# Kernel tuning notes

Measured on AMD Instinct MI355X. Metric: run time of the kernel, lower is better.

Reference implementation:

```python
import jax, jax.numpy as jnp
import numpy as np

L, B, E, H = 2048, 2, 1024, 16
D = E // H
R = E // 4  # self-space subspace rank
ALPHA = 0.6


def setup_inputs() -> dict:
    key = jax.random.key(0)
    ks = jax.random.split(key, 11)
    s = 0.02
    return {
        "x": jax.random.normal(ks[0], (L, B, E), jnp.float32),
        "attn_mask": jnp.zeros((L, L), jnp.float32),
        "Wq": jax.random.normal(ks[1], (E, E), jnp.float32) * s,
        "bq": jnp.zeros((E,), jnp.float32),
        "Wk": jax.random.normal(ks[2], (E, E), jnp.float32) * s,
        "bk": jnp.zeros((E,), jnp.float32),
        "Wv": jax.random.normal(ks[3], (E, E), jnp.float32) * s,
        "bv": jnp.zeros((E,), jnp.float32),
        "Wo": jax.random.normal(ks[4], (E, E), jnp.float32) * s,
        "bo": jnp.zeros((E,), jnp.float32),
        "U": jax.random.normal(ks[5], (E, R), jnp.float32) * (1.0 / np.sqrt(E)),
    }


def _condition(t, U):
    # self_space.condition: blend with projection onto learned subspace U
    # t: [..., E]
    return ALPHA * t + (1.0 - ALPHA) * ((t @ U) @ U.T)


def reference(x, attn_mask, Wq, bq, Wk, bk, Wv, bv, Wo, bo, U):
    # x: [L, B, E] (seq-first)
    Q = x @ Wq.T + bq
    K = x @ Wk.T + bk
    V = x @ Wv.T + bv
    Qc = _condition(Q, U)
    Kc = _condition(K, U)
    # split heads: [L, B, H, D]
    q = Qc.reshape(L, B, H, D)
    k = Kc.reshape(L, B, H, D)
    v = V.reshape(L, B, H, D)
    scores = jnp.einsum("lbhd,mbhd->bhlm", q, k) / jnp.sqrt(jnp.float32(D))
    scores = scores + attn_mask  # broadcast [L,L] over [B,H,L,L]
    attn_weights = jax.nn.softmax(scores, axis=-1)  # dropout p=0.0 -> identity
    ctx = jnp.einsum("bhlm,mbhd->lbhd", attn_weights, v).reshape(L, B, E)
    out = ctx @ Wo.T + bo
    return out, attn_weights  # attn_weights: [B, H, L, L]
```

## Files before the change

kernel.cpp:

```cpp
#include <hip/hip_runtime.h>
#include <cstddef>

#define L_SEQ  2048
#define B_SZ   2
#define E_DIM  1024
#define H_N    16
#define D_HEAD 64
#define R_DIM  256

typedef unsigned short u16;
using bf16x8 = __attribute__((ext_vector_type(8))) short;
using f32x4  = __attribute__((ext_vector_type(4))) float;

__device__ __forceinline__ u16 bf16rne(float f) {
    unsigned u = __float_as_uint(f);
    return (u16)((u + 0x7FFFu + ((u >> 16) & 1u)) >> 16);
}
__device__ __forceinline__ float b2f(u16 h) {
    return __uint_as_float(((unsigned)h) << 16);
}

__global__ __launch_bounds__(256)
void convert_hilo(const float* __restrict__ in, u16* __restrict__ hi,
                  u16* __restrict__ lo, int n4)
{
    for (int i = blockIdx.x * 256 + threadIdx.x; i < n4; i += gridDim.x * 256) {
        float4 v = ((const float4*)in)[i];
        u16 h0 = bf16rne(v.x), h1 = bf16rne(v.y), h2 = bf16rne(v.z), h3 = bf16rne(v.w);
        uint2 hp;
        hp.x = (unsigned)h0 | ((unsigned)h1 << 16);
        hp.y = (unsigned)h2 | ((unsigned)h3 << 16);
        ((uint2*)hi)[i] = hp;
        u16 l0 = bf16rne(v.x - b2f(h0)), l1 = bf16rne(v.y - b2f(h1));
        u16 l2 = bf16rne(v.z - b2f(h2)), l3 = bf16rne(v.w - b2f(h3));
        uint2 lp;
        lp.x = (unsigned)l0 | ((unsigned)l1 << 16);
        lp.y = (unsigned)l2 | ((unsigned)l3 << 16);
        ((uint2*)lo)[i] = lp;
    }
}

__global__ __launch_bounds__(256)
void transpose_f32_hilo(const float* __restrict__ in, u16* __restrict__ oh,
                        u16* __restrict__ ol, int rows, int cols)
{
    __shared__ float t[32][33];
    const int tx = threadIdx.x & 31, ty = threadIdx.x >> 5;
    const int r0 = blockIdx.y * 32, c0 = blockIdx.x * 32;
    #pragma unroll
    for (int i = 0; i < 4; i++)
        t[ty + i * 8][tx] = in[(size_t)(r0 + ty + i * 8) * cols + c0 + tx];
    __syncthreads();
    #pragma unroll
    for (int i = 0; i < 4; i++) {
        float v = t[tx][ty + i * 8];
        u16 h = bf16rne(v);
        size_t o = (size_t)(c0 + ty + i * 8) * rows + r0 + tx;
        oh[o] = h;
        ol[o] = bf16rne(v - b2f(h));
    }
}

__global__ __launch_bounds__(256)
void transpose_v_bf16(const u16* __restrict__ vh, u16* __restrict__ vt)
{
    __shared__ u16 t[32][34];
    const int tx = threadIdx.x & 31, ty = threadIdx.x >> 5;
    const int l0 = blockIdx.x * 32, d0 = blockIdx.y * 32;
    const int z = blockIdx.z, b = z >> 4, h = z & 15;
    #pragma unroll
    for (int i = 0; i < 4; i++)
        t[ty + i * 8][tx] =
            vh[(size_t)((l0 + ty + i * 8) * B_SZ + b) * E_DIM + h * D_HEAD + d0 + tx];
    __syncthreads();
    #pragma unroll
    for (int i = 0; i < 4; i++)
        vt[(size_t)(z * D_HEAD + d0 + ty + i * 8) * L_SEQ + l0 + tx] = t[tx][ty + i * 8];
}

__global__ void flag_init(int* f) { if (threadIdx.x == 0) *f = 0; }

__global__ __launch_bounds__(256)
void mask_scan(const float* __restrict__ m, int* __restrict__ f, int n4)
{
    int nz = 0;
    for (int i = blockIdx.x * 256 + threadIdx.x; i < n4; i += gridDim.x * 256) {
        float4 v = ((const float4*)m)[i];
        nz |= (v.x != 0.0f) | (v.y != 0.0f) | (v.z != 0.0f) | (v.w != 0.0f);
    }
    if (nz) atomicOr(f, 1);
}

template <int BN, bool SPLIT, bool AF32>
__global__ __launch_bounds__(256)
void gemm_mfma(const void* __restrict__ Ah_, const void* __restrict__ Al_,
               const u16* __restrict__ Bh_, const u16* __restrict__ Bl_,
               float* __restrict__ Cf, u16* __restrict__ Ch, u16* __restrict__ Cl,
               const u16* __restrict__ Cinh, const u16* __restrict__ Cinl,
               const float* __restrict__ bias,
               int M, int N, int K, int lda, int ldb, int ldc,
               long aStride, int aMode, long bStride, int bMode,
               long cStride, int cMode, float alpha, float beta)
{
    constexpr int BM = 128, BK = 64;
    constexpr int WN = BN / 32;
    constexpr int ALO = BM * BK, BLO = BN * BK;
    __shared__ __align__(16) u16 As[(SPLIT ? 2 : 1) * BM * BK];
    __shared__ __align__(16) u16 Bs[(SPLIT ? 2 : 1) * BN * BK];

    const int tid = threadIdx.x;
    const int z = blockIdx.z;
    const int headOff = (z >> 4) * E_DIM + (z & 15) * D_HEAD;
    const int aOff = aMode ? headOff : (int)(z * aStride);
    const int bOff = bMode ? headOff : (int)(z * bStride);
    const int cOff = cMode ? headOff : (int)(z * cStride);
    const int tm = blockIdx.y * BM, tn = blockIdx.x * BN;

    const int sRow = tid >> 3, sG = tid & 7;
    const int lane = tid & 63;
    const int fr = lane & 15, kg = lane >> 4;
    const int wave = tid >> 6;
    const int wm = (wave >> 1) * 64;
    const int wn = (wave & 1) * (BN / 2);

    f32x4 acc[4][WN] = {};

    for (int k0 = 0; k0 < K; k0 += BK) {
        if constexpr (!AF32) {
            const u16* Ah = (const u16*)Ah_ + aOff + k0;
            #pragma unroll
            for (int i = 0; i < 4; i++) {
                int row = sRow + i * 32;
                int p = sG ^ (row & 7);
                int dst = row * BK + p * 8;
                *(uint4*)&As[dst] = *(const uint4*)(Ah + (tm + row) * lda + sG * 8);
                if constexpr (SPLIT) {
                    const u16* Al = (const u16*)Al_ + aOff + k0;
                    *(uint4*)&As[ALO + dst] = *(const uint4*)(Al + (tm + row) * lda + sG * 8);
                }
            }
        } else {
            const float* Af = (const float*)Ah_ + aOff + k0;
            const int rowF = tid >> 4, qF = tid & 15;
            #pragma unroll
            for (int i = 0; i < 8; i++) {
                int row = rowF + i * 16;
                float4 v = *(const float4*)(Af + (long)(tm + row) * lda + qF * 4);
                int p = (qF >> 1) ^ (row & 7);
                uint2 pk;
                pk.x = (unsigned)bf16rne(v.x) | ((unsigned)bf16rne(v.y) << 16);
                pk.y = (unsigned)bf16rne(v.z) | ((unsigned)bf16rne(v.w) << 16);
                *(uint2*)&As[row * BK + p * 8 + (qF & 1) * 4] = pk;
            }
        }
        {
            const u16* Bh = Bh_ + bOff + k0;
            #pragma unroll
            for (int i = 0; i < BN / 32; i++) {
                int row = sRow + i * 32;
                int p = sG ^ (row & 7);
                int dst = row * BK + p * 8;
                *(uint4*)&Bs[dst] = *(const uint4*)(Bh + (tn + row) * ldb + sG * 8);
                if constexpr (SPLIT) {
                    const u16* Bl = Bl_ + bOff + k0;
                    *(uint4*)&Bs[BLO + dst] = *(const uint4*)(Bl + (tn + row) * ldb + sG * 8);
                }
            }
        }
        __syncthreads();

        #pragma unroll
        for (int ks = 0; ks < 2; ks++) {
            bf16x8 ah[4], al[4];
            #pragma unroll
            for (int m = 0; m < 4; m++) {
                int row = wm + m * 16 + fr;
                int p = (ks * 4 + kg) ^ (row & 7);
                ah[m] = *(const bf16x8*)&As[row * BK + p * 8];
                if constexpr (SPLIT)
                    al[m] = *(const bf16x8*)&As[ALO + row * BK + p * 8];
            }
            #pragma unroll
            for (int n = 0; n < WN; n++) {
                int col = wn + n * 16 + fr;
                int p = (ks * 4 + kg) ^ (col & 7);
                bf16x8 bh = *(const bf16x8*)&Bs[col * BK + p * 8];
                #pragma unroll
                for (int m = 0; m < 4; m++)
                    acc[m][n] = __builtin_amdgcn_mfma_f32_16x16x32_bf16(ah[m], bh, acc[m][n], 0, 0, 0);
                if constexpr (SPLIT) {
                    bf16x8 bl = *(const bf16x8*)&Bs[BLO + col * BK + p * 8];
                    #pragma unroll
                    for (int m = 0; m < 4; m++) {
                        acc[m][n] = __builtin_amdgcn_mfma_f32_16x16x32_bf16(al[m], bh, acc[m][n], 0, 0, 0);
                        acc[m][n] = __builtin_amdgcn_mfma_f32_16x16x32_bf16(ah[m], bl, acc[m][n], 0, 0, 0);
                    }
                }
            }
        }
        __syncthreads();
    }

    #pragma unroll
    for (int m = 0; m < 4; m++) {
        int row0 = tm + wm + m * 16 + kg * 4;
        #pragma unroll
        for (int n = 0; n < WN; n++) {
            int col = tn + wn + n * 16 + fr;
            float bv = bias ? bias[col] : 0.0f;
            #pragma unroll
            for (int j = 0; j < 4; j++) {
                int idx = cOff + (row0 + j) * ldc + col;
                float v = alpha * acc[m][n][j] + bv;
                if (beta != 0.0f) {
                    float ci = b2f(Cinh[idx]);
                    if (Cinl) ci += b2f(Cinl[idx]);
                    v += beta * ci;
                }
                if (Cf) Cf[idx] = v;
                if (Ch) {
                    u16 h = bf16rne(v);
                    Ch[idx] = h;
                    if (Cl) Cl[idx] = bf16rne(v - b2f(h));
                }
            }
        }
    }
}

__global__ __launch_bounds__(256)
void attn_fused(const u16* __restrict__ Qc, const u16* __restrict__ Kc,
                const u16* __restrict__ Vt, float* __restrict__ attn,
                u16* __restrict__ ctxh, u16* __restrict__ ctxl,
                const float* __restrict__ mask, const int* __restrict__ maskFlag)
{
    __shared__ __align__(16) u16 Qs[64 * 64];
    __shared__ __align__(16) u16 Ks[64 * 64];
    __shared__ __align__(16) u16 Vs[64 * 64];
    __shared__ __align__(16) u16 Ps[4][16 * 64];

    const int tid = threadIdx.x;
    const int z  = blockIdx.y;
    const int q0 = blockIdx.x * 64;
    const int qkOff = (z >> 4) * E_DIM + (z & 15) * D_HEAD;
    const long vtOff = (long)z * D_HEAD * L_SEQ;
    const long aOff  = (long)z * L_SEQ * L_SEQ;
    const int ldq = B_SZ * E_DIM;

    const int lane = tid & 63;
    const int fr = lane & 15, kg = lane >> 4;
    const int wave = tid >> 6;
    const int wq = wave * 16;

    const bool useMask = maskFlag[0] != 0;
    const int sR = tid >> 3, sG = tid & 7;

    #pragma unroll
    for (int i = 0; i < 2; i++) {
        int row = sR + i * 32;
        *(uint4*)&Qs[row * 64 + (sG ^ (row & 7)) * 8] =
            *(const uint4*)(Qc + (long)(q0 + row) * ldq + qkOff + sG * 8);
    }
    __syncthreads();
    bf16x8 qf[2];
    #pragma unroll
    for (int ks = 0; ks < 2; ks++) {
        int row = wq + fr;
        qf[ks] = *(const bf16x8*)&Qs[row * 64 + ((ks * 4 + kg) ^ (row & 7)) * 8];
    }
    __syncthreads();

    float mrow[4], lrow[4];
    #pragma unroll
    for (int j = 0; j < 4; j++) { mrow[j] = -3.4e38f; lrow[j] = 0.0f; }

    for (int kt = 0; kt < L_SEQ / 64; kt++) {
        const int kv0 = kt * 64;
        #pragma unroll
        for (int i = 0; i < 2; i++) {
            int row = sR + i * 32;
            *(uint4*)&Ks[row * 64 + (sG ^ (row & 7)) * 8] =
                *(const uint4*)(Kc + (long)(kv0 + row) * ldq + qkOff + sG * 8);
        }
        __syncthreads();

        f32x4 acc[4] = {};
        #pragma unroll
        for (int ks = 0; ks < 2; ks++) {
            #pragma unroll
            for (int n = 0; n < 4; n++) {
                int col = n * 16 + fr;
                bf16x8 bh = *(const bf16x8*)&Ks[col * 64 + ((ks * 4 + kg) ^ (col & 7)) * 8];
                acc[n] = __builtin_amdgcn_mfma_f32_16x16x32_bf16(qf[ks], bh, acc[n], 0, 0, 0);
            }
        }
        __syncthreads();

        #pragma unroll
        for (int j = 0; j < 4; j++) {
            float v[4];
            #pragma unroll
            for (int n = 0; n < 4; n++) {
                v[n] = acc[n][j] * 0.125f;
                if (useMask)
                    v[n] += mask[(size_t)(q0 + wq + kg * 4 + j) * L_SEQ + kv0 + n * 16 + fr];
            }
            float t0 = fmaxf(fmaxf(v[0], v[1]), fmaxf(v[2], v[3]));
            float nm = fmaxf(mrow[j], t0);
            float sc = __expf(mrow[j] - nm);
            float s  = __expf(v[0] - nm) + __expf(v[1] - nm)
                     + __expf(v[2] - nm) + __expf(v[3] - nm);
            lrow[j] = lrow[j] * sc + s;
            mrow[j] = nm;
        }
    }

    #pragma unroll
    for (int j = 0; j < 4; j++) {
        float m_ = mrow[j], l_ = lrow[j];
        #pragma unroll
        for (int off = 1; off < 16; off <<= 1) {
            float mo = __shfl_xor(m_, off, 64);
            float lo2 = __shfl_xor(l_, off, 64);
            float M = fmaxf(m_, mo);
            l_ = l_ * __expf(m_ - M) + lo2 * __expf(mo - M);
            m_ = M;
        }
        mrow[j] = m_;
        lrow[j] = 1.0f / l_;
    }

    u16* Pw = &Ps[wave][0];
    f32x4 acc_o[4] = {};

    for (int kt = 0; kt < L_SEQ / 64; kt++) {
        const int kv0 = kt * 64;
        #pragma unroll
        for (int i = 0; i < 2; i++) {
            int row = sR + i * 32;
            *(uint4*)&Ks[row * 64 + (sG ^ (row & 7)) * 8] =
                *(const uint4*)(Kc + (long)(kv0 + row) * ldq + qkOff + sG * 8);
            *(uint4*)&Vs[row * 64 + (sG ^ (row & 7)) * 8] =
                *(const uint4*)(Vt + vtOff + (long)row * L_SEQ + kv0 + sG * 8);
        }
        __syncthreads();

        f32x4 acc[4] = {};
        #pragma unroll
        for (int ks = 0; ks < 2; ks++) {
            #pragma unroll
            for (int n = 0; n < 4; n++) {
                int col = n * 16 + fr;
                bf16x8 bh = *(const bf16x8*)&Ks[col * 64 + ((ks * 4 + kg) ^ (col & 7)) * 8];
                acc[n] = __builtin_amdgcn_mfma_f32_16x16x32_bf16(qf[ks], bh, acc[n], 0, 0, 0);
            }
        }

        #pragma unroll
        for (int n = 0; n < 4; n++) {
            #pragma unroll
            for (int j = 0; j < 4; j++) {
                int row = kg * 4 + j;
                int col = n * 16 + fr;
                float v = acc[n][j] * 0.125f;
                if (useMask)
                    v += mask[(size_t)(q0 + wq + row) * L_SEQ + kv0 + col];
                float p = __expf(v - mrow[j]) * lrow[j];
                attn[aOff + (size_t)(q0 + wq + row) * L_SEQ + kv0 + col] = p;
                Pw[row * 64 + ((col >> 3) ^ (row & 7)) * 8 + (col & 7)] = bf16rne(p);
            }
        }

        asm volatile("" ::: "memory");

        #pragma unroll
        for (int ks = 0; ks < 2; ks++) {
            int rowA = fr;
            bf16x8 pa = *(const bf16x8*)&Pw[rowA * 64 + ((ks * 4 + kg) ^ (rowA & 7)) * 8];
            #pragma unroll
            for (int n = 0; n < 4; n++) {
                int d = n * 16 + fr;
                bf16x8 vb = *(const bf16x8*)&Vs[d * 64 + ((ks * 4 + kg) ^ (d & 7)) * 8];
                acc_o[n] = __builtin_amdgcn_mfma_f32_16x16x32_bf16(pa, vb, acc_o[n], 0, 0, 0);
            }
        }
        __syncthreads();
    }

    #pragma unroll
    for (int n = 0; n < 4; n++) {
        #pragma unroll
        for (int j = 0; j < 4; j++) {
            int row = q0 + wq + kg * 4 + j;
            int d = n * 16 + fr;
            float v = acc_o[n][j];
            size_t idx = (size_t)row * ldq + qkOff + d;
            u16 h = bf16rne(v);
            ctxh[idx] = h;
            ctxl[idx] = bf16rne(v - b2f(h));
        }
    }
}

extern "C" void kernel_launch(void* const* d_in, const int* in_sizes, int n_in,
                              void* d_out, int out_size, void* d_ws, size_t ws_size,
                              hipStream_t stream)
{
    const float* x    = (const float*)d_in[0];
    const float* mask = (const float*)d_in[1];
    const float* Wq   = (const float*)d_in[2];
    const float* bq   = (const float*)d_in[3];
    const float* Wk   = (const float*)d_in[4];
    const float* bk   = (const float*)d_in[5];
    const float* Wv   = (const float*)d_in[6];
    const float* bv   = (const float*)d_in[7];
    const float* Wo   = (const float*)d_in[8];
    const float* bo   = (const float*)d_in[9];
    const float* U    = (const float*)d_in[10];

    float* out   = (float*)d_out;
    float* attnF = out + (size_t)L_SEQ * B_SZ * E_DIM;

    const int SZ  = L_SEQ * B_SZ * E_DIM;
    const int WSZ = E_DIM * E_DIM;
    const int USZ = E_DIM * R_DIM;
    const int PSZ = L_SEQ * B_SZ * R_DIM;

    u16* Qch  = (u16*)d_ws;
    u16* Kch  = Qch + SZ;
    u16* Vth  = Kch + SZ;
    u16* ctxh = Vth + SZ;
    u16* ctxl = ctxh + SZ;
    u16* Woh  = ctxl + SZ;
    u16* Wol  = Woh + WSZ;
    int* maskFlag = (int*)(Wol + WSZ);

    u16* sc  = (u16*)attnF;
    u16* xh  = sc;          u16* xl  = xh + SZ;
    u16* Qh  = xl + SZ;     u16* Ql  = Qh + SZ;
    u16* Kh  = Ql + SZ;     u16* Kl  = Kh + SZ;
    u16* Vh  = Kl + SZ;
    u16* Wqh = Vh + SZ;     u16* Wql = Wqh + WSZ;
    u16* Wkh = Wql + WSZ;   u16* Wkl = Wkh + WSZ;
    u16* Wvh = Wkl + WSZ;   u16* Wvl = Wvh + WSZ;
    u16* Uh  = Wvl + WSZ;   u16* Ul  = Uh + USZ;
    u16* Uth = Ul + USZ;    u16* Utl = Uth + USZ;
    u16* Ph  = Utl + USZ;   u16* Pl  = Ph + PSZ;

    const dim3 blk(256);
    const int M = L_SEQ * B_SZ;

    hipLaunchKernelGGL(flag_init, dim3(1), dim3(64), 0, stream, maskFlag);
    hipLaunchKernelGGL(mask_scan, dim3(512), blk, 0, stream,
                       mask, maskFlag, (L_SEQ * L_SEQ) / 4);

    hipLaunchKernelGGL(convert_hilo, dim3(2048), blk, 0, stream, x,  xh,  xl,  SZ / 4);
    hipLaunchKernelGGL(convert_hilo, dim3(512),  blk, 0, stream, Wq, Wqh, Wql, WSZ / 4);
    hipLaunchKernelGGL(convert_hilo, dim3(512),  blk, 0, stream, Wk, Wkh, Wkl, WSZ / 4);
    hipLaunchKernelGGL(convert_hilo, dim3(512),  blk, 0, stream, Wv, Wvh, Wvl, WSZ / 4);
    hipLaunchKernelGGL(convert_hilo, dim3(512),  blk, 0, stream, Wo, Woh, Wol, WSZ / 4);
    hipLaunchKernelGGL(convert_hilo, dim3(128),  blk, 0, stream, U,  Uh,  Ul,  USZ / 4);
    hipLaunchKernelGGL(transpose_f32_hilo, dim3(R_DIM / 32, E_DIM / 32), blk, 0, stream,
                       U, Uth, Utl, E_DIM, R_DIM);

    {
        dim3 g(E_DIM / 128, M / 128, 1);
        hipLaunchKernelGGL((gemm_mfma<128, true, false>), g, blk, 0, stream,
            xh, xl, Wqh, Wql, nullptr, Qh, Ql, nullptr, nullptr, bq,
            M, E_DIM, E_DIM, E_DIM, E_DIM, E_DIM,
            0L, 0, 0L, 0, 0L, 0, 1.0f, 0.0f);
        hipLaunchKernelGGL((gemm_mfma<128, true, false>), g, blk, 0, stream,
            xh, xl, Wkh, Wkl, nullptr, Kh, Kl, nullptr, nullptr, bk,
            M, E_DIM, E_DIM, E_DIM, E_DIM, E_DIM,
            0L, 0, 0L, 0, 0L, 0, 1.0f, 0.0f);
        hipLaunchKernelGGL((gemm_mfma<128, true, false>), g, blk, 0, stream,
            xh, xl, Wvh, Wvl, nullptr, Vh, nullptr, nullptr, nullptr, bv,
            M, E_DIM, E_DIM, E_DIM, E_DIM, E_DIM,
            0L, 0, 0L, 0, 0L, 0, 1.0f, 0.0f);
    }
    hipLaunchKernelGGL(transpose_v_bf16, dim3(L_SEQ / 32, D_HEAD / 32, B_SZ * H_N),
                       blk, 0, stream, Vh, Vth);

    {
        dim3 gp(R_DIM / 128, M / 128, 1);
        dim3 gc(E_DIM / 128, M / 128, 1);
        hipLaunchKernelGGL((gemm_mfma<128, true, false>), gp, blk, 0, stream,
            Qh, Ql, Uth, Utl, nullptr, Ph, Pl, nullptr, nullptr, nullptr,
            M, R_DIM, E_DIM, E_DIM, E_DIM, R_DIM,
            0L, 0, 0L, 0, 0L, 0, 1.0f, 0.0f);
        hipLaunchKernelGGL((gemm_mfma<128, true, false>), gc, blk, 0, stream,
            Ph, Pl, Uh, Ul, nullptr, Qch, nullptr, Qh, Ql, nullptr,
            M, E_DIM, R_DIM, R_DIM, R_DIM, E_DIM,
            0L, 0, 0L, 0, 0L, 0, 0.4f, 0.6f);
        hipLaunchKernelGGL((gemm_mfma<128, true, false>), gp, blk, 0, stream,
            Kh, Kl, Uth, Utl, nullptr, Ph, Pl, nullptr, nullptr, nullptr,
            M, R_DIM, E_DIM, E_DIM, E_DIM, R_DIM,
            0L, 0, 0L, 0, 0L, 0, 1.0f, 0.0f);
        hipLaunchKernelGGL((gemm_mfma<128, true, false>), gc, blk, 0, stream,
            Ph, Pl, Uh, Ul, nullptr, Kch, nullptr, Kh, Kl, nullptr,
            M, E_DIM, R_DIM, R_DIM, R_DIM, E_DIM,
            0L, 0, 0L, 0, 0L, 0, 0.4f, 0.6f);
    }

    hipLaunchKernelGGL(attn_fused, dim3(L_SEQ / 64, B_SZ * H_N), blk, 0, stream,
                       Qch, Kch, Vth, attnF, ctxh, ctxl, mask, maskFlag);

    {
        dim3 g(E_DIM / 128, M / 128, 1);
        hipLaunchKernelGGL((gemm_mfma<128, true, false>), g, blk, 0, stream,
            ctxh, ctxl, Woh, Wol, out, nullptr, nullptr, nullptr, nullptr, bo,
            M, E_DIM, E_DIM, E_DIM, E_DIM, E_DIM,
            0L, 0, 0L, 0, 0L, 0, 1.0f, 0.0f);
    }
}
```

Baseline: 1.084 ms.

## Fold subspace conditioning into Q/K weights and use direct global-to-LDS loads

Uses linearity to precompute conditioned weights (0.6*W + 0.4*U(U^T W)) and biases, so the Q and K projections come out already conditioned. This removes the four per-activation rank-R GEMMs and the Q/K hi/lo intermediates, at the cost of extra weight-sized transposes and GEMMs on every call. It also switches GEMM and attention tile loads to global_load_lds with a lane-XOR swizzle, which skips the register staging step. Rounding of the folded weights differs slightly from the original order of operations.

```diff
diff --git a/kernel.cpp b/kernel.cpp
--- a/kernel.cpp
+++ b/kernel.cpp
@@ -18,6 +18,12 @@
 }
 __device__ __forceinline__ float b2f(u16 h) {
     return __uint_as_float(((unsigned)h) << 16);
+}
+
+__device__ __forceinline__ void gload16(const u16* g, u16* l) {
+    __builtin_amdgcn_global_load_lds(
+        (const __attribute__((address_space(1))) void*)g,
+        (__attribute__((address_space(3))) void*)l, 16, 0, 0);
 }
 
 __global__ __launch_bounds__(256)
@@ -91,80 +97,62 @@
     if (nz) atomicOr(f, 1);
 }
 
-template <int BN, bool SPLIT, bool AF32>
-__global__ __launch_bounds__(256)
-void gemm_mfma(const void* __restrict__ Ah_, const void* __restrict__ Al_,
-               const u16* __restrict__ Bh_, const u16* __restrict__ Bl_,
+__global__ __launch_bounds__(256)
+void bias_fold1(const float* __restrict__ b, const float* __restrict__ U,
+                float* __restrict__ tmp)
+{
+    const int r = threadIdx.x;
+    float s = 0.0f;
+    for (int e = 0; e < E_DIM; e++) s += U[(size_t)e * R_DIM + r] * b[e];
+    tmp[r] = s;
+}
+
+__global__ __launch_bounds__(256)
+void bias_fold2(const float* __restrict__ b, const float* __restrict__ U,
+                const float* __restrict__ tmp, float* __restrict__ beff)
+{
+    const int e = blockIdx.x * 256 + threadIdx.x;
+    float s = 0.0f;
+    for (int r = 0; r < R_DIM; r++) s += U[(size_t)e * R_DIM + r] * tmp[r];
+    beff[e] = 0.6f * b[e] + 0.4f * s;
+}
+
+template <bool SPLIT>
+__global__ __launch_bounds__(256)
+void gemm_mfma(const u16* __restrict__ Ah, const u16* __restrict__ Al,
+               const u16* __restrict__ Bh, const u16* __restrict__ Bl,
                float* __restrict__ Cf, u16* __restrict__ Ch, u16* __restrict__ Cl,
                const u16* __restrict__ Cinh, const u16* __restrict__ Cinl,
                const float* __restrict__ bias,
                int M, int N, int K, int lda, int ldb, int ldc,
-               long aStride, int aMode, long bStride, int bMode,
-               long cStride, int cMode, float alpha, float beta)
-{
-    constexpr int BM = 128, BK = 64;
-    constexpr int WN = BN / 32;
+               float alpha, float beta)
+{
+    constexpr int BM = 128, BN = 128, BK = 64;
     constexpr int ALO = BM * BK, BLO = BN * BK;
     __shared__ __align__(16) u16 As[(SPLIT ? 2 : 1) * BM * BK];
     __shared__ __align__(16) u16 Bs[(SPLIT ? 2 : 1) * BN * BK];
 
     const int tid = threadIdx.x;
-    const int z = blockIdx.z;
-    const int headOff = (z >> 4) * E_DIM + (z & 15) * D_HEAD;
-    const int aOff = aMode ? headOff : (int)(z * aStride);
-    const int bOff = bMode ? headOff : (int)(z * bStride);
-    const int cOff = cMode ? headOff : (int)(z * cStride);
     const int tm = blockIdx.y * BM, tn = blockIdx.x * BN;
-
-    const int sRow = tid >> 3, sG = tid & 7;
     const int lane = tid & 63;
     const int fr = lane & 15, kg = lane >> 4;
     const int wave = tid >> 6;
-    const int wm = (wave >> 1) * 64;
-    const int wn = (wave & 1) * (BN / 2);
-
-    f32x4 acc[4][WN] = {};
+    const int wm = (wave >> 1) * 64, wn = (wave & 1) * 64;
+
+    const int sR8 = lane >> 3;
+    const int sG  = ((lane & 7) ^ sR8) * 8;
+
+    f32x4 acc[4][4] = {};
 
     for (int k0 = 0; k0 < K; k0 += BK) {
-        if constexpr (!AF32) {
-            const u16* Ah = (const u16*)Ah_ + aOff + k0;
-            #pragma unroll
-            for (int i = 0; i < 4; i++) {
-                int row = sRow + i * 32;
-                int p = sG ^ (row & 7);
-                int dst = row * BK + p * 8;
-                *(uint4*)&As[dst] = *(const uint4*)(Ah + (tm + row) * lda + sG * 8);
-                if constexpr (SPLIT) {
-                    const u16* Al = (const u16*)Al_ + aOff + k0;
-                    *(uint4*)&As[ALO + dst] = *(const uint4*)(Al + (tm + row) * lda + sG * 8);
-                }
-            }
-        } else {
-            const float* Af = (const float*)Ah_ + aOff + k0;
-            const int rowF = tid >> 4, qF = tid & 15;
-            #pragma unroll
-            for (int i = 0; i < 8; i++) {
-                int row = rowF + i * 16;
-                float4 v = *(const float4*)(Af + (long)(tm + row) * lda + qF * 4);
-                int p = (qF >> 1) ^ (row & 7);
-                uint2 pk;
-                pk.x = (unsigned)bf16rne(v.x) | ((unsigned)bf16rne(v.y) << 16);
-                pk.y = (unsigned)bf16rne(v.z) | ((unsigned)bf16rne(v.w) << 16);
-                *(uint2*)&As[row * BK + p * 8 + (qF & 1) * 4] = pk;
-            }
-        }
-        {
-            const u16* Bh = Bh_ + bOff + k0;
-            #pragma unroll
-            for (int i = 0; i < BN / 32; i++) {
-                int row = sRow + i * 32;
-                int p = sG ^ (row & 7);
-                int dst = row * BK + p * 8;
-                *(uint4*)&Bs[dst] = *(const uint4*)(Bh + (tn + row) * ldb + sG * 8);
-                if constexpr (SPLIT) {
-                    const u16* Bl = Bl_ + bOff + k0;
-                    *(uint4*)&Bs[BLO + dst] = *(const uint4*)(Bl + (tn + row) * ldb + sG * 8);
-                }
+        #pragma unroll
+        for (int c = 0; c < 4; c++) {
+            const int r0 = (c * 4 + wave) * 8;
+            gload16(Ah + (size_t)(tm + r0 + sR8) * lda + k0 + sG, &As[r0 * BK]);
+            gload16(Bh + (size_t)(tn + r0 + sR8) * ldb + k0 + sG, &Bs[r0 * BK]);
+            if constexpr (SPLIT) {
+                gload16(Al + (size_t)(tm + r0 + sR8) * lda + k0 + sG, &As[ALO + r0 * BK]);
+                gload16(Bl + (size_t)(tn + r0 + sR8) * ldb + k0 + sG, &Bs[BLO + r0 * BK]);
             }
         }
         __syncthreads();
@@ -181,7 +169,7 @@
                     al[m] = *(const bf16x8*)&As[ALO + row * BK + p * 8];
             }
             #pragma unroll
-            for (int n = 0; n < WN; n++) {
+            for (int n = 0; n < 4; n++) {
                 int col = wn + n * 16 + fr;
                 int p = (ks * 4 + kg) ^ (col & 7);
                 bf16x8 bh = *(const bf16x8*)&Bs[col * BK + p * 8];
@@ -205,12 +193,12 @@
     for (int m = 0; m < 4; m++) {
         int row0 = tm + wm + m * 16 + kg * 4;
         #pragma unroll
-        for (int n = 0; n < WN; n++) {
+        for (int n = 0; n < 4; n++) {
             int col = tn + wn + n * 16 + fr;
             float bv = bias ? bias[col] : 0.0f;
             #pragma unroll
             for (int j = 0; j < 4; j++) {
-                int idx = cOff + (row0 + j) * ldc + col;
+                size_t idx = (size_t)(row0 + j) * ldc + col;
                 float v = alpha * acc[m][n][j] + bv;
                 if (beta != 0.0f) {
                     float ci = b2f(Cinh[idx]);
@@ -253,13 +241,13 @@
     const int wq = wave * 16;
 
     const bool useMask = maskFlag[0] != 0;
-    const int sR = tid >> 3, sG = tid & 7;
-
-    #pragma unroll
-    for (int i = 0; i < 2; i++) {
-        int row = sR + i * 32;
-        *(uint4*)&Qs[row * 64 + (sG ^ (row & 7)) * 8] =
-            *(const uint4*)(Qc + (long)(q0 + row) * ldq + qkOff + sG * 8);
+    const int sR8 = lane >> 3;
+    const int sG  = ((lane & 7) ^ sR8) * 8;
+
+    #pragma unroll
+    for (int c = 0; c < 2; c++) {
+        const int r0 = (c * 4 + wave) * 8;
+        gload16(Qc + (size_t)(q0 + r0 + sR8) * ldq + qkOff + sG, &Qs[r0 * 64]);
     }
     __syncthreads();
     bf16x8 qf[2];
@@ -277,10 +265,9 @@
     for (int kt = 0; kt < L_SEQ / 64; kt++) {
         const int kv0 = kt * 64;
         #pragma unroll
-        for (int i = 0; i < 2; i++) {
-            int row = sR + i * 32;
-            *(uint4*)&Ks[row * 64 + (sG ^ (row & 7)) * 8] =
-                *(const uint4*)(Kc + (long)(kv0 + row) * ldq + qkOff + sG * 8);
+        for (int c = 0; c < 2; c++) {
+            const int r0 = (c * 4 + wave) * 8;
+            gload16(Kc + (size_t)(kv0 + r0 + sR8) * ldq + qkOff + sG, &Ks[r0 * 64]);
         }
         __syncthreads();
 
@@ -336,12 +323,10 @@
     for (int kt = 0; kt < L_SEQ / 64; kt++) {
         const int kv0 = kt * 64;
         #pragma unroll
-        for (int i = 0; i < 2; i++) {
-            int row = sR + i * 32;
-            *(uint4*)&Ks[row * 64 + (sG ^ (row & 7)) * 8] =
-                *(const uint4*)(Kc + (long)(kv0 + row) * ldq + qkOff + sG * 8);
-            *(uint4*)&Vs[row * 64 + (sG ^ (row & 7)) * 8] =
-                *(const uint4*)(Vt + vtOff + (long)row * L_SEQ + kv0 + sG * 8);
+        for (int c = 0; c < 2; c++) {
+            const int r0 = (c * 4 + wave) * 8;
+            gload16(Kc + (size_t)(kv0 + r0 + sR8) * ldq + qkOff + sG, &Ks[r0 * 64]);
+            gload16(Vt + vtOff + (size_t)(r0 + sR8) * L_SEQ + kv0 + sG, &Vs[r0 * 64]);
         }
         __syncthreads();
 
@@ -424,7 +409,6 @@
     const int SZ  = L_SEQ * B_SZ * E_DIM;
     const int WSZ = E_DIM * E_DIM;
     const int USZ = E_DIM * R_DIM;
-    const int PSZ = L_SEQ * B_SZ * R_DIM;
 
     u16* Qch  = (u16*)d_ws;
     u16* Kch  = Qch + SZ;
@@ -435,17 +419,23 @@
     u16* Wol  = Woh + WSZ;
     int* maskFlag = (int*)(Wol + WSZ);
 
-    u16* sc  = (u16*)attnF;
-    u16* xh  = sc;          u16* xl  = xh + SZ;
-    u16* Qh  = xl + SZ;     u16* Ql  = Qh + SZ;
-    u16* Kh  = Ql + SZ;     u16* Kl  = Kh + SZ;
-    u16* Vh  = Kl + SZ;
-    u16* Wqh = Vh + SZ;     u16* Wql = Wqh + WSZ;
-    u16* Wkh = Wql + WSZ;   u16* Wkl = Wkh + WSZ;
-    u16* Wvh = Wkl + WSZ;   u16* Wvl = Wvh + WSZ;
-    u16* Uh  = Wvl + WSZ;   u16* Ul  = Uh + USZ;
-    u16* Uth = Ul + USZ;    u16* Utl = Uth + USZ;
-    u16* Ph  = Utl + USZ;   u16* Pl  = Ph + PSZ;
+    u16* sc   = (u16*)attnF;
+    u16* xh   = sc;          u16* xl   = xh + SZ;
+    u16* Wqh  = xl + SZ;     u16* Wql  = Wqh + WSZ;
+    u16* Wkh  = Wql + WSZ;   u16* Wkl  = Wkh + WSZ;
+    u16* Wvh  = Wkl + WSZ;   u16* Wvl  = Wvh + WSZ;
+    u16* Uh   = Wvl + WSZ;   u16* Ul   = Uh + USZ;
+    u16* Uth  = Ul + USZ;    u16* Utl  = Uth + USZ;
+    u16* WqTh = Utl + USZ;   u16* WqTl = WqTh + WSZ;
+    u16* WkTh = WqTl + WSZ;  u16* WkTl = WkTh + WSZ;
+    u16* GTqh = WkTl + WSZ;  u16* GTql = GTqh + USZ;
+    u16* GTkh = GTql + USZ;  u16* GTkl = GTkh + USZ;
+    u16* Wfqh = GTkl + USZ;  u16* Wfql = Wfqh + WSZ;
+    u16* Wfkh = Wfql + WSZ;  u16* Wfkl = Wfkh + WSZ;
+    u16* Vh   = Wfkl + WSZ;
+    float* bqe  = (float*)(Vh + SZ);
+    float* bke  = bqe + E_DIM;
+    float* tmpv = bke + E_DIM;
 
     const dim3 blk(256);
     const int M = L_SEQ * B_SZ;
@@ -462,54 +452,55 @@
     hipLaunchKernelGGL(convert_hilo, dim3(128),  blk, 0, stream, U,  Uh,  Ul,  USZ / 4);
     hipLaunchKernelGGL(transpose_f32_hilo, dim3(R_DIM / 32, E_DIM / 32), blk, 0, stream,
                        U, Uth, Utl, E_DIM, R_DIM);
+    hipLaunchKernelGGL(transpose_f32_hilo, dim3(E_DIM / 32, E_DIM / 32), blk, 0, stream,
+                       Wq, WqTh, WqTl, E_DIM, E_DIM);
+    hipLaunchKernelGGL(transpose_f32_hilo, dim3(E_DIM / 32, E_DIM / 32), blk, 0, stream,
+                       Wk, WkTh, WkTl, E_DIM, E_DIM);
+
+    hipLaunchKernelGGL(bias_fold1, dim3(1), blk, 0, stream, bq, U, tmpv);
+    hipLaunchKernelGGL(bias_fold2, dim3(E_DIM / 256), blk, 0, stream, bq, U, tmpv, bqe);
+    hipLaunchKernelGGL(bias_fold1, dim3(1), blk, 0, stream, bk, U, tmpv);
+    hipLaunchKernelGGL(bias_fold2, dim3(E_DIM / 256), blk, 0, stream, bk, U, tmpv, bke);
+
+    {
+        dim3 gt(R_DIM / 128, E_DIM / 128, 1);
+        dim3 gw(E_DIM / 128, E_DIM / 128, 1);
+        hipLaunchKernelGGL((gemm_mfma<true>), gt, blk, 0, stream,
+            WqTh, WqTl, Uth, Utl, nullptr, GTqh, GTql, nullptr, nullptr, nullptr,
+            E_DIM, R_DIM, E_DIM, E_DIM, E_DIM, R_DIM, 1.0f, 0.0f);
+        hipLaunchKernelGGL((gemm_mfma<true>), gw, blk, 0, stream,
+            Uh, Ul, GTqh, GTql, nullptr, Wfqh, Wfql, Wqh, Wql, nullptr,
+            E_DIM, E_DIM, R_DIM, R_DIM, R_DIM, E_DIM, 0.4f, 0.6f);
+        hipLaunchKernelGGL((gemm_mfma<true>), gt, blk, 0, stream,
+            WkTh, WkTl, Uth, Utl, nullptr, GTkh, GTkl, nullptr, nullptr, nullptr,
+            E_DIM, R_DIM, E_DIM, E_DIM, E_DIM, R_DIM, 1.0f, 0.0f);
+        hipLaunchKernelGGL((gemm_mfma<true>), gw, blk, 0, stream,
+            Uh, Ul, GTkh, GTkl, nullptr, Wfkh, Wfkl, Wkh, Wkl, nullptr,
+            E_DIM, E_DIM, R_DIM, R_DIM, R_DIM, E_DIM, 0.4f, 0.6f);
+    }
 
     {
         dim3 g(E_DIM / 128, M / 128, 1);
-        hipLaunchKernelGGL((gemm_mfma<128, true, false>), g, blk, 0, stream,
-            xh, xl, Wqh, Wql, nullptr, Qh, Ql, nullptr, nullptr, bq,
-            M, E_DIM, E_DIM, E_DIM, E_DIM, E_DIM,
-            0L, 0, 0L, 0, 0L, 0, 1.0f, 0.0f);
-        hipLaunchKernelGGL((gemm_mfma<128, true, false>), g, blk, 0, stream,
-            xh, xl, Wkh, Wkl, nullptr, Kh, Kl, nullptr, nullptr, bk,
-            M, E_DIM, E_DIM, E_DIM, E_DIM, E_DIM,
-            0L, 0, 0L, 0, 0L, 0, 1.0f, 0.0f);
-        hipLaunchKernelGGL((gemm_mfma<128, true, false>), g, blk, 0, stream,
+        hipLaunchKernelGGL((gemm_mfma<true>), g, blk, 0, stream,
+            xh, xl, Wfqh, Wfql, nullptr, Qch, nullptr, nullptr, nullptr, bqe,
+            M, E_DIM, E_DIM, E_DIM, E_DIM, E_DIM, 1.0f, 0.0f);
+        hipLaunchKernelGGL((gemm_mfma<true>), g, blk, 0, stream,
+            xh, xl, Wfkh, Wfkl, nullptr, Kch, nullptr, nullptr, nullptr, bke,
+            M, E_DIM, E_DIM, E_DIM, E_DIM, E_DIM, 1.0f, 0.0f);
+        hipLaunchKernelGGL((gemm_mfma<true>), g, blk, 0, stream,
             xh, xl, Wvh, Wvl, nullptr, Vh, nullptr, nullptr, nullptr, bv,
-            M, E_DIM, E_DIM, E_DIM, E_DIM, E_DIM,
-            0L, 0, 0L, 0, 0L, 0, 1.0f, 0.0f);
+            M, E_DIM, E_DIM, E_DIM, E_DIM, E_DIM, 1.0f, 0.0f);
     }
     hipLaunchKernelGGL(transpose_v_bf16, dim3(L_SEQ / 32, D_HEAD / 32, B_SZ * H_N),
                        blk, 0, stream, Vh, Vth);
 
-    {
-        dim3 gp(R_DIM / 128, M / 128, 1);
-        dim3 gc(E_DIM / 128, M / 128, 1);
-        hipLaunchKernelGGL((gemm_mfma<128, true, false>), gp, blk, 0, stream,
-            Qh, Ql, Uth, Utl, nullptr, Ph, Pl, nullptr, nullptr, nullptr,
-            M, R_DIM, E_DIM, E_DIM, E_DIM, R_DIM,
-            0L, 0, 0L, 0, 0L, 0, 1.0f, 0.0f);
-        hipLaunchKernelGGL((gemm_mfma<128, true, false>), gc, blk, 0, stream,
-            Ph, Pl, Uh, Ul, nullptr, Qch, nullptr, Qh, Ql, nullptr,
-            M, E_DIM, R_DIM, R_DIM, R_DIM, E_DIM,
-            0L, 0, 0L, 0, 0L, 0, 0.4f, 0.6f);
-        hipLaunchKernelGGL((gemm_mfma<128, true, false>), gp, blk, 0, stream,
-            Kh, Kl, Uth, Utl, nullptr, Ph, Pl, nullptr, nullptr, nullptr,
-            M, R_DIM, E_DIM, E_DIM, E_DIM, R_DIM,
-            0L, 0, 0L, 0, 0L, 0, 1.0f, 0.0f);
-        hipLaunchKernelGGL((gemm_mfma<128, true, false>), gc, blk, 0, stream,
-            Ph, Pl, Uh, Ul, nullptr, Kch, nullptr, Kh, Kl, nullptr,
-            M, E_DIM, R_DIM, R_DIM, R_DIM, E_DIM,
-            0L, 0, 0L, 0, 0L, 0, 0.4f, 0.6f);
-    }
-
     hipLaunchKernelGGL(attn_fused, dim3(L_SEQ / 64, B_SZ * H_N), blk, 0, stream,
                        Qch, Kch, Vth, attnF, ctxh, ctxl, mask, maskFlag);
 
     {
         dim3 g(E_DIM / 128, M / 128, 1);
-        hipLaunchKernelGGL((gemm_mfma<128, true, false>), g, blk, 0, stream,
+        hipLaunchKernelGGL((gemm_mfma<true>), g, blk, 0, stream,
             ctxh, ctxl, Woh, Wol, out, nullptr, nullptr, nullptr, nullptr, bo,
-            M, E_DIM, E_DIM, E_DIM, E_DIM, E_DIM,
-            0L, 0, 0L, 0, 0L, 0, 1.0f, 0.0f);
-    }
-}
+            M, E_DIM, E_DIM, E_DIM, E_DIM, E_DIM, 1.0f, 0.0f);
+    }
+}
```

Measured after the change: 1.151 ms. 1.06x slower.
